# Kernel tuning notes

Measured on AMD Instinct MI355X. Metric: run time of the kernel, lower is better.

## Reference

```python
import jax, jax.numpy as jnp
import numpy as np

HEADS = 8

def _conv(x, w, b, stride, pad):
    # x: [B,C,H,W], w: [O,I,kh,kw] (torch OIHW layout)
    y = jax.lax.conv_general_dilated(x, w, (stride, stride), ((pad, pad), (pad, pad)),
                                     dimension_numbers=('NCHW', 'OIHW', 'NCHW'))
    return y + b[None, :, None, None]

def _maxpool2x2(x):
    # returns pooled values and one-hot argmax per 2x2 window (torch first-max tie-break)
    b, c, H, W = x.shape
    win = x.reshape(b, c, H // 2, 2, W // 2, 2).transpose(0, 1, 2, 4, 3, 5).reshape(b, c, H // 2, W // 2, 4)
    am = jnp.argmax(win, axis=-1)
    oh = jax.nn.one_hot(am, 4, dtype=x.dtype)
    pooled = jnp.sum(win * oh, axis=-1)
    return pooled, oh

def _maxunpool2x2(y, oh):
    b, c, h2, w2 = y.shape
    out = y[..., None] * oh  # [b,c,h2,w2,4]
    out = out.reshape(b, c, h2, w2, 2, 2).transpose(0, 1, 2, 4, 3, 5).reshape(b, c, h2 * 2, w2 * 2)
    return out

def _mha2d(x, wq, wk, wv, wo):
    # x: [b,c,h,w]; wq/wk/wv/wo stored as [in,out] so y = x @ W
    b, c, h, w = x.shape
    hw = h * w
    dk = wq.shape[1]
    dh = dk // HEADS
    xt = x.reshape(b, c, hw).transpose(0, 2, 1)  # [b,hw,c]
    def split(y):  # torch: view(b,hw,dh,heads).permute(0,3,1,2)
        return y.reshape(b, hw, dh, HEADS).transpose(0, 3, 1, 2)  # [b,heads,hw,dh]
    q = split(xt @ wq)
    k = split(xt @ wk)
    v = split(xt @ wv)
    scale = jnp.sqrt(jnp.asarray(dh, x.dtype))
    attn = jax.nn.softmax(jnp.einsum('bhqd,bhkd->bhqk', q, k) / scale, axis=-1)
    o = jnp.einsum('bhqk,bhkd->bhqd', attn, v)
    o = o.transpose(0, 2, 3, 1).reshape(b, hw, dk)  # [b,hw,dh,heads] -> merge
    o = o @ wo
    return o.transpose(0, 2, 1).reshape(b, dk, h, w)

def setup_inputs() -> dict:
    key = jax.random.key(0)
    ks = jax.random.split(key, 10)
    B, C, H, W = 16, 256, 64, 64
    s = 0.05
    return {
        'x': jax.random.normal(ks[0], (B, C, H, W), jnp.float32),
        'conv_w': jax.random.normal(ks[1], (C, C, 3, 3), jnp.float32) * s,
        'conv_b': jax.random.normal(ks[2], (C,), jnp.float32) * s,
        'fr_w': jax.random.normal(ks[3], (C, C, 1, 1), jnp.float32) * s,
        'fr_b': jax.random.normal(ks[4], (C,), jnp.float32) * s,
        'wq': jax.random.normal(ks[5], (C, C), jnp.float32) * s,
        'wk': jax.random.normal(ks[6], (C, C), jnp.float32) * s,
        'wv': jax.random.normal(ks[7], (C, C), jnp.float32) * s,
        'wo': jax.random.normal(ks[8], (C, C), jnp.float32) * s,
        'gamma': jax.random.normal(ks[9], (1,), jnp.float32) * 0.1,
    }

def reference(x, conv_w, conv_b, fr_w, fr_b, wq, wk, wv, wo, gamma):
    _x = _conv(x, fr_w, fr_b, 1, 0)          # 1x1 feature reduction
    _x, oh = _maxpool2x2(_x)                 # MaxPool2d(2, return_indices=True)
    _x = _mha2d(_x, wq, wk, wv, wo)          # attention over pooled grid
    _x = _maxunpool2x2(_x, oh)               # MaxUnpool2d(2)
    return _x * jnp.tanh(gamma[0]) + _conv(x, conv_w, conv_b, 1, 1)
```

## Files before the change

### kernel.cpp

```cpp
#include <hip/hip_runtime.h>
#include <hip/hip_bf16.h>
#include <math.h>

#define B 16
#define C 256
#define H 64
#define W 64
#define H2 32
#define W2 32
#define HW2 1024
#define HEADS 8
#define DH 32

typedef unsigned short ushort_t;
using short8 = __attribute__((ext_vector_type(8))) short;
using u16x8  = __attribute__((ext_vector_type(8))) unsigned short;
using f32x4  = __attribute__((ext_vector_type(4))) float;

__device__ inline ushort_t f2bf(float f) {
    __hip_bfloat16 hb = __float2bfloat16(f);
    return *(ushort_t*)&hb;
}
__device__ inline float bf2f(ushort_t u) {
    return __uint_as_float(((unsigned)u) << 16);
}

__device__ __forceinline__ void cp16(const ushort_t* g, ushort_t* l) {
    __builtin_amdgcn_global_load_lds(
        (const __attribute__((address_space(1))) void*)g,
        (__attribute__((address_space(3))) void*)l, 16, 0, 0);
}

#define RSCALE 0.17677669529663687f

__global__ __launch_bounds__(256) void k_prep_wT(const float* __restrict__ cw,
                                                 ushort_t* __restrict__ wbfT) {
    int i = threadIdx.x, o = blockIdx.x;
    const float* src = cw + ((size_t)o * C + i) * 9;
#pragma unroll
    for (int kk = 0; kk < 9; kk++)
        wbfT[((size_t)kk * C + o) * C + i] = f2bf(src[kk]);
}

__global__ __launch_bounds__(256) void k_prep_wx(
    const float* __restrict__ wq, const float* __restrict__ wk,
    const float* __restrict__ wv, const float* __restrict__ wo,
    const float* __restrict__ frw, ushort_t* __restrict__ wqkvT,
    ushort_t* __restrict__ woT, ushort_t* __restrict__ wfr) {
    int op = blockIdx.x, mat = blockIdx.y, t = threadIdx.x;
    if (mat < 3) {
        const float* w = (mat == 0) ? wq : (mat == 1) ? wk : wv;
        int hh = op >> 5, d = op & 31, col = d * 8 + hh;
        wqkvT[(size_t)mat * 65536 + op * 256 + t] = f2bf(w[t * 256 + col]);
    } else if (mat == 3) {
        int hh = t >> 5, d = t & 31, ic = d * 8 + hh;
        woT[op * 256 + t] = f2bf(wo[ic * 256 + op]);
    } else {
        wfr[op * 256 + t] = f2bf(frw[op * 256 + t]);
    }
}

__global__ __launch_bounds__(256) void k_prep_xn(const float* __restrict__ x,
                                                 ushort_t* __restrict__ xn) {
    __shared__ ushort_t ldsT[64 * 258];
    int t = threadIdx.x;
    int hp = blockIdx.x, b = blockIdx.y;
    ushort_t* dst = xn + ((size_t)(b * 66 + hp)) * 66 * 256;

    if (hp == 0 || hp == 65) {
        u16x8 z = (u16x8){0, 0, 0, 0, 0, 0, 0, 0};
        for (int i = t; i < 2112; i += 256) *(u16x8*)(dst + i * 8) = z;
        return;
    }
    const float* xb = x + ((size_t)b * 256) * 4096 + (size_t)(hp - 1) * 64;
    {
        int cq = t >> 6, w = t & 63;
#pragma unroll 8
        for (int it = 0; it < 64; ++it) {
            int c = it * 4 + cq;
            float v = xb[(size_t)c * 4096 + w];
            ldsT[w * 258 + c] = f2bf(v);
        }
    }
    __syncthreads();
    {
        u16x8 z = (u16x8){0, 0, 0, 0, 0, 0, 0, 0};
        if (t < 32) *(u16x8*)(dst + t * 8) = z;
        else if (t < 64) *(u16x8*)(dst + 65 * 256 + (t - 32) * 8) = z;
    }
    {
        int half = t >> 7, cl = t & 127;
#pragma unroll 4
        for (int it = 0; it < 32; ++it) {
            int w = it * 2 + half;
            unsigned v = *(const unsigned*)&ldsT[w * 258 + cl * 2];
            *(unsigned*)(dst + (size_t)(w + 1) * 256 + cl * 2) = v;
        }
    }
}

__global__ __launch_bounds__(256) void k_conv1pool_mfma(
    const ushort_t* __restrict__ xn, const ushort_t* __restrict__ wfr,
    const float* __restrict__ frb, ushort_t* __restrict__ Pbf,
    unsigned char* __restrict__ idx) {
    __shared__ __align__(16) ushort_t sh[32768];
    ushort_t* Als = sh;
    ushort_t* Bls = sh + 8192;
    int t = threadIdx.x;
    int wg = blockIdx.x;
    int mt = (wg & 7) * 64 + (wg >> 3);
    int b = mt >> 5;
    int h0 = (mt * 2) & 63;

    int r = t >> 2, p = t & 3;
    int kswz = (p ^ ((r >> 1) & 3)) * 8;
    const ushort_t* aB0 = xn + ((size_t)((b * 66 + h0 + 1) * 66 + (r + 1))) * 256 + kswz;
    const ushort_t* aB1 = xn + ((size_t)((b * 66 + h0 + 2) * 66 + (r + 1))) * 256 + kswz;
    const ushort_t* bB = wfr + (size_t)r * 256 + kswz;

    f32x4 acc[4][8];
#pragma unroll
    for (int mf = 0; mf < 4; mf++)
#pragma unroll
        for (int nf = 0; nf < 8; nf++) acc[mf][nf] = (f32x4){0.f, 0.f, 0.f, 0.f};

    cp16(aB0, &Als[t * 8]);
    cp16(aB1, &Als[2048 + t * 8]);
    cp16(bB, &Bls[t * 8]);
    cp16(bB + 64 * 256, &Bls[2048 + t * 8]);
    cp16(bB + 128 * 256, &Bls[4096 + t * 8]);
    cp16(bB + 192 * 256, &Bls[6144 + t * 8]);
    __syncthreads();

    int l = t & 63, wid = t >> 6, wm = wid >> 1, wn = wid & 1;
    int arow = wm * 64 + (l & 15);
    int brow = wn * 128 + (l & 15);
    int pslot = ((l >> 4) ^ ((l >> 1) & 3)) * 8;

    for (int s = 0; s < 8; s++) {
        int cur = s & 1;
        if (s < 7) {
            int off = (s + 1) * 32;
            int nb = cur ^ 1;
            cp16(aB0 + off, &Als[nb * 4096 + t * 8]);
            cp16(aB1 + off, &Als[nb * 4096 + 2048 + t * 8]);
            cp16(bB + off, &Bls[nb * 8192 + t * 8]);
            cp16(bB + 64 * 256 + off, &Bls[nb * 8192 + 2048 + t * 8]);
            cp16(bB + 128 * 256 + off, &Bls[nb * 8192 + 4096 + t * 8]);
            cp16(bB + 192 * 256 + off, &Bls[nb * 8192 + 6144 + t * 8]);
        }
        short8 af[4], bf[8];
#pragma unroll
        for (int mf = 0; mf < 4; mf++)
            af[mf] = *(const short8*)&Als[cur * 4096 + (arow + mf * 16) * 32 + pslot];
#pragma unroll
        for (int nf = 0; nf < 8; nf++)
            bf[nf] = *(const short8*)&Bls[cur * 8192 + (brow + nf * 16) * 32 + pslot];
#pragma unroll
        for (int mf = 0; mf < 4; mf++)
#pragma unroll
            for (int nf = 0; nf < 8; nf++)
                acc[mf][nf] = __builtin_amdgcn_mfma_f32_16x16x32_bf16(
                    af[mf], bf[nf], acc[mf][nf], 0, 0, 0);
        __syncthreads();
    }

#pragma unroll
    for (int nf = 0; nf < 8; nf++) {
        int o = wn * 128 + nf * 16 + (l & 15);
        float bias = frb[o];
#pragma unroll
        for (int mf = 0; mf < 4; mf++) {
            int rbase = wm * 64 + mf * 16 + ((l >> 4) << 2);
            f32x4 a = acc[mf][nf];
#pragma unroll
            for (int jj = 0; jj < 4; jj++)
                sh[(rbase + jj) * 256 + o] = f2bf(a[jj] + bias);
        }
    }
    __syncthreads();

    {
        int h2 = mt & 31;
        size_t rowb = (size_t)(b << 10) + h2 * 32;
        int o0 = (t & 31) * 8;
#pragma unroll
        for (int pp = 0; pp < 4; pp++) {
            int w2 = pp * 8 + (t >> 5);
            u16x8 r0 = *(const u16x8*)&sh[(2 * w2) * 256 + o0];
            u16x8 r1 = *(const u16x8*)&sh[(2 * w2 + 1) * 256 + o0];
            u16x8 r2 = *(const u16x8*)&sh[(64 + 2 * w2) * 256 + o0];
            u16x8 r3 = *(const u16x8*)&sh[(64 + 2 * w2 + 1) * 256 + o0];
            u16x8 pv;
            unsigned amlo = 0, amhi = 0;
#pragma unroll
            for (int e = 0; e < 8; e++) {
                float v0 = bf2f(r0[e]), v1 = bf2f(r1[e]);
                float v2 = bf2f(r2[e]), v3 = bf2f(r3[e]);
                float m = v0;
                ushort_t raw = r0[e];
                unsigned am = 0;
                if (v1 > m) { m = v1; raw = r1[e]; am = 1; }
                if (v2 > m) { m = v2; raw = r2[e]; am = 2; }
                if (v3 > m) { m = v3; raw = r3[e]; am = 3; }
                pv[e] = raw;
                if (e < 4) amlo |= am << (8 * e);
                else       amhi |= am << (8 * (e - 4));
            }
            size_t po = (rowb + w2) * 256 + o0;
            *(u16x8*)(Pbf + po) = pv;
            *(uint2*)(idx + po) = make_uint2(amlo, amhi);
        }
    }
}

__global__ __launch_bounds__(256) void k_qkv_mfma(
    const ushort_t* __restrict__ A, const ushort_t* __restrict__ Bw,
    ushort_t* __restrict__ qb, ushort_t* __restrict__ kb,
    ushort_t* __restrict__ vtb) {
    __shared__ __align__(16) ushort_t Als[2][4096];
    __shared__ __align__(16) ushort_t Bls[2][4096];
    int t = threadIdx.x;
    int wg = blockIdx.x;
    int linear = (wg & 7) * 96 + (wg >> 3);
    int mt = linear / 6, nt = linear % 6;

    int r = t >> 2, p = t & 3;
    int kswz = (p ^ ((r >> 1) & 3)) * 8;
    const ushort_t* aB0 = A + ((size_t)(mt * 128 + r)) * 256 + kswz;
    const ushort_t* aB1 = aB0 + (size_t)64 * 256;
    const ushort_t* bB0 = Bw + ((size_t)(nt * 128 + r)) * 256 + kswz;
    const ushort_t* bB1 = bB0 + (size_t)64 * 256;

    f32x4 acc[4][4];
#pragma unroll
    for (int mf = 0; mf < 4; mf++)
#pragma unroll
        for (int nf = 0; nf < 4; nf++) acc[mf][nf] = (f32x4){0.f, 0.f, 0.f, 0.f};

    cp16(aB0, &Als[0][t * 8]);
    cp16(aB1, &Als[0][2048 + t * 8]);
    cp16(bB0, &Bls[0][t * 8]);
    cp16(bB1, &Bls[0][2048 + t * 8]);
    __syncthreads();

    int l = t & 63, wid = t >> 6, wm = wid >> 1, wn = wid & 1;
    int arow = wm * 64 + (l & 15);
    int brow = wn * 64 + (l & 15);
    int pslot = ((l >> 4) ^ ((l >> 1) & 3)) * 8;

    for (int s = 0; s < 8; s++) {
        int cur = s & 1;
        if (s < 7) {
            int off = (s + 1) * 32;
            int nb = cur ^ 1;
            cp16(aB0 + off, &Als[nb][t * 8]);
            cp16(aB1 + off, &Als[nb][2048 + t * 8]);
            cp16(bB0 + off, &Bls[nb][t * 8]);
            cp16(bB1 + off, &Bls[nb][2048 + t * 8]);
        }
        short8 af[4], bf[4];
#pragma unroll
        for (int mf = 0; mf < 4; mf++)
            af[mf] = *(const short8*)&Als[cur][(arow + mf * 16) * 32 + pslot];
#pragma unroll
        for (int nf = 0; nf < 4; nf++)
            bf[nf] = *(const short8*)&Bls[cur][(brow + nf * 16) * 32 + pslot];
#pragma unroll
        for (int mf = 0; mf < 4; mf++)
#pragma unroll
            for (int nf = 0; nf < 4; nf++)
                acc[mf][nf] = __builtin_amdgcn_mfma_f32_16x16x32_bf16(
                    af[mf], bf[nf], acc[mf][nf], 0, 0, 0);
        __syncthreads();
    }

    if (nt < 4) {
        ushort_t* dst = (nt < 2) ? qb : kb;
        float sc = (nt < 2) ? RSCALE : 1.0f;
        int ccb = (nt & 1) * 128 + wn * 64;
#pragma unroll
        for (int nf = 0; nf < 4; nf++) {
            int cc = ccb + nf * 16 + (l & 15);
#pragma unroll
            for (int mf = 0; mf < 4; mf++) {
                int m = mt * 128 + wm * 64 + mf * 16 + ((l >> 4) << 2);
                f32x4 a = acc[mf][nf];
#pragma unroll
                for (int jj = 0; jj < 4; jj++)
                    dst[(size_t)(m + jj) * 256 + cc] = f2bf(a[jj] * sc);
            }
        }
    } else {
#pragma unroll
        for (int nf = 0; nf < 4; nf++) {
            int cc = (nt & 1) * 128 + wn * 64 + nf * 16 + (l & 15);
#pragma unroll
            for (int mf = 0; mf < 4; mf++) {
                int m = mt * 128 + wm * 64 + mf * 16 + ((l >> 4) << 2);
                int b = m >> 10, n0 = m & 1023;
                f32x4 a = acc[mf][nf];
                unsigned u0 = ((unsigned)f2bf(a[1]) << 16) | f2bf(a[0]);
                unsigned u1 = ((unsigned)f2bf(a[3]) << 16) | f2bf(a[2]);
                *(uint2*)&vtb[((size_t)(b * 256 + cc)) * 1024 + n0] =
                    make_uint2(u0, u1);
            }
        }
    }
}

__global__ __launch_bounds__(256) void k_attn_mfma(
    const ushort_t* __restrict__ qb, const ushort_t* __restrict__ kb,
    const ushort_t* __restrict__ vtb, ushort_t* __restrict__ aoT) {
    __shared__ __align__(16) ushort_t Klds[2][2048];
    __shared__ __align__(16) ushort_t Vlds[2][2048];
    __shared__ __align__(16) ushort_t Plds[4][2304];
    __shared__ float rs_lds[128];

    int t = threadIdx.x;
    int bid = blockIdx.x;
    int swz = (bid & 7) * 128 + (bid >> 3);
    int bh = swz >> 3, qt = swz & 7;
    int b = bh >> 3, h = bh & 7;
    int w = t >> 6, l = t & 63, g = l >> 4, li = l & 15;

    size_t qrow = (size_t)(b * 1024 + qt * 128 + w * 32 + li);
    short8 qv0 = *(const short8*)(qb + qrow * 256 + h * 32 + g * 8);
    short8 qv1 = *(const short8*)(qb + (qrow + 16) * 256 + h * 32 + g * 8);

    int sr = t >> 2, sp = t & 3;
    const ushort_t* kg =
        kb + ((size_t)(b * 1024 + sr)) * 256 + h * 32 + ((sp ^ ((sr >> 1) & 3)) * 8);
    int vd = t >> 3, vs = t & 7;
    const ushort_t* vg =
        vtb + ((size_t)(b * 256 + h * 32 + vd)) * 1024 + ((vs ^ (vd & 7)) * 8);

    f32x4 oacc[2][2];
    f32x4 rsv[2];
#pragma unroll
    for (int qf = 0; qf < 2; qf++) {
        rsv[qf] = (f32x4){0.f, 0.f, 0.f, 0.f};
#pragma unroll
        for (int df = 0; df < 2; df++) oacc[qf][df] = (f32x4){0.f, 0.f, 0.f, 0.f};
    }

    cp16(kg, &Klds[0][t * 8]);
    cp16(vg, &Vlds[0][t * 8]);
    __syncthreads();

    ushort_t* Pw = &Plds[w][0];

    for (int c = 0; c < 16; c++) {
        int cur = c & 1;
        if (c < 15) {
            cp16(kg + (size_t)(c + 1) * 64 * 256, &Klds[cur ^ 1][t * 8]);
            cp16(vg + (c + 1) * 64, &Vlds[cur ^ 1][t * 8]);
        }
        short8 ak[4];
#pragma unroll
        for (int kf = 0; kf < 4; kf++)
            ak[kf] = *(const short8*)&Klds[cur][(16 * kf + li) * 32 +
                                               ((g ^ ((l >> 1) & 3)) * 8)];
#pragma unroll
        for (int qf = 0; qf < 2; qf++) {
            short8 qv = qf ? qv1 : qv0;
#pragma unroll
            for (int kf = 0; kf < 4; kf++) {
                f32x4 st = __builtin_amdgcn_mfma_f32_16x16x32_bf16(
                    ak[kf], qv, (f32x4){0.f, 0.f, 0.f, 0.f}, 0, 0, 0);
                float p0 = __expf(st[0]), p1 = __expf(st[1]);
                float p2 = __expf(st[2]), p3 = __expf(st[3]);
                rsv[qf][0] += p0; rsv[qf][1] += p1;
                rsv[qf][2] += p2; rsv[qf][3] += p3;
                unsigned u0, u1;
                asm("v_cvt_pk_bf16_f32 %0, %1, %2" : "=v"(u0) : "v"(p0), "v"(p1));
                asm("v_cvt_pk_bf16_f32 %0, %1, %2" : "=v"(u1) : "v"(p2), "v"(p3));
                *(uint2*)&Pw[(16 * qf + li) * 72 + 16 * kf + 4 * g] =
                    make_uint2(u0, u1);
            }
        }
#pragma unroll
        for (int win = 0; win < 2; win++) {
            short8 pa[2], bv[2];
#pragma unroll
            for (int qf = 0; qf < 2; qf++)
                pa[qf] = *(const short8*)&Pw[(16 * qf + li) * 72 + win * 32 + 8 * g];
#pragma unroll
            for (int df = 0; df < 2; df++)
                bv[df] = *(const short8*)&Vlds[cur][(16 * df + li) * 64 +
                                                    (((win * 4 + g) ^ (l & 7)) * 8)];
#pragma unroll
            for (int qf = 0; qf < 2; qf++)
#pragma unroll
                for (int df = 0; df < 2; df++)
                    oacc[qf][df] = __builtin_amdgcn_mfma_f32_16x16x32_bf16(
                        pa[qf], bv[df], oacc[qf][df], 0, 0, 0);
        }
        __syncthreads();
    }

#pragma unroll
    for (int qf = 0; qf < 2; qf++) {
        float rs = (rsv[qf][0] + rsv[qf][1]) + (rsv[qf][2] + rsv[qf][3]);
        rs += __shfl_xor(rs, 16);
        rs += __shfl_xor(rs, 32);
        if (l < 16) rs_lds[w * 32 + 16 * qf + li] = rs;
    }
    __syncthreads();

#pragma unroll
    for (int qf = 0; qf < 2; qf++) {
        float4 rs4 = *(const float4*)&rs_lds[w * 32 + 16 * qf + 4 * g];
        float inv[4] = {1.f / rs4.x, 1.f / rs4.y, 1.f / rs4.z, 1.f / rs4.w};
#pragma unroll
        for (int df = 0; df < 2; df++) {
            f32x4 a = oacc[qf][df];
#pragma unroll
            for (int r2 = 0; r2 < 4; r2++) {
                size_t row = (size_t)(b * 1024 + qt * 128 + w * 32 + 16 * qf +
                                      4 * g + r2);
                aoT[row * 256 + h * 32 + 16 * df + li] = f2bf(a[r2] * inv[r2]);
            }
        }
    }
}

__global__ __launch_bounds__(256) void k_oproj_mfma(
    const ushort_t* __restrict__ A, const ushort_t* __restrict__ Bw,
    float* __restrict__ y2) {
    __shared__ __align__(16) ushort_t Als[2][4096];
    __shared__ __align__(16) ushort_t Bls[2][4096];
    int t = threadIdx.x;
    int wg = blockIdx.x;
    int linear = (wg & 7) * 32 + (wg >> 3);
    int nt = linear & 1, mt = linear >> 1;

    int r = t >> 2, p = t & 3;
    int kswz = (p ^ ((r >> 1) & 3)) * 8;
    const ushort_t* aB0 = A + ((size_t)(mt * 128 + r)) * 256 + kswz;
    const ushort_t* aB1 = aB0 + (size_t)64 * 256;
    const ushort_t* bB0 = Bw + ((size_t)(nt * 128 + r)) * 256 + kswz;
    const ushort_t* bB1 = bB0 + (size_t)64 * 256;

    f32x4 acc[4][4];
#pragma unroll
    for (int mf = 0; mf < 4; mf++)
#pragma unroll
        for (int nf = 0; nf < 4; nf++) acc[mf][nf] = (f32x4){0.f, 0.f, 0.f, 0.f};

    cp16(aB0, &Als[0][t * 8]);
    cp16(aB1, &Als[0][2048 + t * 8]);
    cp16(bB0, &Bls[0][t * 8]);
    cp16(bB1, &Bls[0][2048 + t * 8]);
    __syncthreads();

    int l = t & 63, wid = t >> 6, wm = wid >> 1, wn = wid & 1;
    int arow = wm * 64 + (l & 15);
    int brow = wn * 64 + (l & 15);
    int pslot = ((l >> 4) ^ ((l >> 1) & 3)) * 8;

    for (int s = 0; s < 8; s++) {
        int cur = s & 1;
        if (s < 7) {
            int off = (s + 1) * 32;
            int nb = cur ^ 1;
            cp16(aB0 + off, &Als[nb][t * 8]);
            cp16(aB1 + off, &Als[nb][2048 + t * 8]);
            cp16(bB0 + off, &Bls[nb][t * 8]);
            cp16(bB1 + off, &Bls[nb][2048 + t * 8]);
        }
        short8 af[4], bf[4];
#pragma unroll
        for (int mf = 0; mf < 4; mf++)
            af[mf] = *(const short8*)&Als[cur][(arow + mf * 16) * 32 + pslot];
#pragma unroll
        for (int nf = 0; nf < 4; nf++)
            bf[nf] = *(const short8*)&Bls[cur][(brow + nf * 16) * 32 + pslot];
#pragma unroll
        for (int mf = 0; mf < 4; mf++)
#pragma unroll
            for (int nf = 0; nf < 4; nf++)
                acc[mf][nf] = __builtin_amdgcn_mfma_f32_16x16x32_bf16(
                    af[mf], bf[nf], acc[mf][nf], 0, 0, 0);
        __syncthreads();
    }

#pragma unroll
    for (int nf = 0; nf < 4; nf++) {
        int cc = nt * 128 + wn * 64 + nf * 16 + (l & 15);
#pragma unroll
        for (int mf = 0; mf < 4; mf++) {
            int m = mt * 128 + wm * 64 + mf * 16 + ((l >> 4) << 2);
            f32x4 a = acc[mf][nf];
#pragma unroll
            for (int jj = 0; jj < 4; jj++)
                y2[(size_t)(m + jj) * 256 + cc] = a[jj];
        }
    }
}

__global__ __launch_bounds__(512) void k_conv3_mfma(
    const ushort_t* __restrict__ xn, const ushort_t* __restrict__ wbfT,
    const float* __restrict__ cb, const float* __restrict__ y2,
    const unsigned char* __restrict__ idx, const float* __restrict__ gamma,
    float* __restrict__ out) {
    extern __shared__ __align__(16) ushort_t lds[];
    ushort_t* AL = lds;
    ushort_t* BL = lds + 32768;
    int t = threadIdx.x;
    int mt = blockIdx.x;

    int srow = t >> 3, sslot = t & 7;
    int kel = (sslot ^ (srow & 7)) * 8;
    const ushort_t* aP[2][2];
    const ushort_t* bP[2][2];
#pragma unroll
    for (int hf = 0; hf < 2; hf++)
#pragma unroll
        for (int j = 0; j < 2; j++) {
            int row = hf * 128 + j * 64 + srow;
            int m = mt * 256 + row;
            int b0 = m >> 12, h0 = (m >> 6) & 63, w0 = m & 63;
            aP[hf][j] = xn + ((size_t)((b0 * 66 + h0) * 66 + w0)) * 256 + kel;
            bP[hf][j] = wbfT + (size_t)row * 256 + kel;
        }

    auto offA = [](int kt) -> int {
        int it = kt / 9, khkw = kt - it * 9;
        int kh = khkw / 3, kw = khkw - kh * 3;
        return (kh * 66 + kw) * 256 + it * 64;
    };
    auto offB = [](int kt) -> int {
        int it = kt / 9, khkw = kt - it * 9;
        return khkw * 65536 + it * 64;
    };
    auto STAGE_A = [&](int bb, int hf, int kt) {
        int o = offA(kt);
        ushort_t* d = AL + bb * 16384 + hf * 8192 + t * 8;
        cp16(aP[hf][0] + o, d);
        cp16(aP[hf][1] + o, d + 4096);
    };
    auto STAGE_B = [&](int bb, int hf, int kt) {
        int o = offB(kt);
        ushort_t* d = BL + bb * 16384 + hf * 8192 + t * 8;
        cp16(bP[hf][0] + o, d);
        cp16(bP[hf][1] + o, d + 4096);
    };

    f32x4 acc[8][4];
#pragma unroll
    for (int mf = 0; mf < 8; mf++)
#pragma unroll
        for (int nf = 0; nf < 4; nf++) acc[mf][nf] = (f32x4){0.f, 0.f, 0.f, 0.f};

    int l = t & 63, wid = t >> 6, wm = wid >> 2, wn = wid & 3;
    int lr = l & 15, g = l >> 4, l7 = l & 7;
    int abase = wm * 8192;
    int bbase = (wn >> 1) * 8192 + (wn & 1) * 4096;

    short8 Xa[4][2], Xb[2][2], Ya[4][2], Yb[2][2];

    auto READF = [&](short8 (&fa)[4][2], short8 (&fb)[2][2],
                     const ushort_t* Ab, const ushort_t* Bb, int ah, int bh) {
#pragma unroll
        for (int mf = 0; mf < 4; mf++)
#pragma unroll
            for (int kk = 0; kk < 2; kk++)
                fa[mf][kk] = *(const short8*)
                    &Ab[(ah * 64 + mf * 16 + lr) * 64 + (((kk * 4 + g) ^ l7) * 8)];
#pragma unroll
        for (int nf = 0; nf < 2; nf++)
#pragma unroll
            for (int kk = 0; kk < 2; kk++)
                fb[nf][kk] = *(const short8*)
                    &Bb[(bh * 32 + nf * 16 + lr) * 64 + (((kk * 4 + g) ^ l7) * 8)];
    };
    auto MFMAQ = [&](short8 (&fa)[4][2], short8 (&fb)[2][2], int mo, int no) {
        __builtin_amdgcn_s_setprio(1);
#pragma unroll
        for (int kk = 0; kk < 2; kk++)
#pragma unroll
            for (int mf = 0; mf < 4; mf++)
#pragma unroll
                for (int nf = 0; nf < 2; nf++)
                    acc[mf + mo][nf + no] = __builtin_amdgcn_mfma_f32_16x16x32_bf16(
                        fa[mf][kk], fb[nf][kk], acc[mf + mo][nf + no], 0, 0, 0);
        __builtin_amdgcn_s_setprio(0);
    };
    auto BARW = [&]() {
        __builtin_amdgcn_sched_barrier(0);
        __builtin_amdgcn_s_barrier();
        __builtin_amdgcn_sched_barrier(0);
    };

    STAGE_A(0, 0, 0); STAGE_A(0, 1, 0); STAGE_B(0, 0, 0); STAGE_B(0, 1, 0);
    asm volatile("s_waitcnt vmcnt(0)" ::: "memory");
    STAGE_B(1, 0, 1); STAGE_B(1, 1, 1);
    __builtin_amdgcn_s_barrier();
    READF(Xa, Xb, AL + abase, BL + bbase, 0, 0);

    for (int kt = 0; kt < 36; kt++) {
        int cur = kt & 1, nxt = cur ^ 1;
        const ushort_t* Ac = AL + cur * 16384 + abase;
        const ushort_t* Bc = BL + cur * 16384 + bbase;
        BARW();
        if (kt < 35) { STAGE_A(nxt, 0, kt + 1); STAGE_A(nxt, 1, kt + 1); }
        READF(Ya, Yb, Ac, Bc, 0, 1);
        MFMAQ(Xa, Xb, 0, 0);
        BARW();
        READF(Xa, Xb, Ac, Bc, 1, 1);
        MFMAQ(Ya, Yb, 0, 2);
        BARW();
        asm volatile("s_waitcnt vmcnt(0)" ::: "memory");
        READF(Ya, Yb, Ac, Bc, 1, 0);
        MFMAQ(Xa, Xb, 4, 2);
        BARW();
        if (kt < 34) { STAGE_B(cur, 0, kt + 2); STAGE_B(cur, 1, kt + 2); }
        if (kt < 35) {
            const ushort_t* An = AL + nxt * 16384 + abase;
            const ushort_t* Bn = BL + nxt * 16384 + bbase;
            READF(Xa, Xb, An, Bn, 0, 0);
        }
        MFMAQ(Ya, Yb, 4, 0);
    }

    float tg = tanhf(gamma[0]);
    int mbase = mt * 256 + wm * 128 + (g << 2);
    int obase = wn * 64 + lr;
#pragma unroll
    for (int nf = 0; nf < 4; nf++) {
        int o = obase + nf * 16;
        float bias = cb[o];
#pragma unroll
        for (int mf = 0; mf < 8; mf++) {
            int m = mbase + mf * 16;
            int b = m >> 12, h = (m >> 6) & 63, w0 = m & 63;
            const unsigned char* idr = idx + ((size_t)(b << 10)) * 256;
            const float* y2r = y2 + ((size_t)(b << 10)) * 256;
            f32x4 a = acc[mf][nf];
            float v4[4];
#pragma unroll
            for (int jj = 0; jj < 4; jj++) {
                int wj = w0 + jj;
                int n2 = ((h >> 1) << 5) + (wj >> 1);
                int j2 = ((h & 1) << 1) + (wj & 1);
                float val = a[jj] + bias;
                if (idr[(size_t)n2 * 256 + o] == (unsigned char)j2)
                    val += tg * y2r[(size_t)n2 * 256 + o];
                v4[jj] = val;
            }
            *(float4*)(out + (((size_t)(b * C + o) * H + h) << 6) + w0) =
                make_float4(v4[0], v4[1], v4[2], v4[3]);
        }
    }
}

extern "C" void kernel_launch(void* const* d_in, const int* in_sizes, int n_in,
                              void* d_out, int out_size, void* d_ws, size_t ws_size,
                              hipStream_t stream) {
    const float* x      = (const float*)d_in[0];
    const float* conv_w = (const float*)d_in[1];
    const float* conv_b = (const float*)d_in[2];
    const float* fr_w   = (const float*)d_in[3];
    const float* fr_b   = (const float*)d_in[4];
    const float* wq     = (const float*)d_in[5];
    const float* wk     = (const float*)d_in[6];
    const float* wv     = (const float*)d_in[7];
    const float* wo     = (const float*)d_in[8];
    const float* gamma  = (const float*)d_in[9];
    float* out = (float*)d_out;
    char* ws = (char*)d_ws;

    ushort_t* wbfT  = (ushort_t*)(ws + 0);
    ushort_t* wfrbf = (ushort_t*)(ws + 1179648);
    ushort_t* wqkvT = (ushort_t*)(ws + 1310720);
    ushort_t* woT   = (ushort_t*)(ws + 1703936);
    ushort_t* xn    = (ushort_t*)(ws + 2097152);
    ushort_t* Pbf   = (ushort_t*)(ws + 37781504);
    unsigned char* idx = (unsigned char*)(ws + 46170112);
    ushort_t* qb    = (ushort_t*)(ws + 50364416);
    ushort_t* kb    = (ushort_t*)(ws + 58753024);
    ushort_t* vtb   = (ushort_t*)(ws + 67141632);
    ushort_t* aoT   = (ushort_t*)(ws + 75530240);
    float* y2       = (float*)(ws + 50364416);

    k_prep_wT<<<dim3(C), dim3(256), 0, stream>>>(conv_w, wbfT);
    k_prep_wx<<<dim3(256, 5), dim3(256), 0, stream>>>(wq, wk, wv, wo, fr_w,
                                                      wqkvT, woT, wfrbf);
    k_prep_xn<<<dim3(66, B), dim3(256), 0, stream>>>(x, xn);
    k_conv1pool_mfma<<<dim3(512), dim3(256), 0, stream>>>(xn, wfrbf, fr_b, Pbf, idx);
    k_qkv_mfma<<<dim3(768), dim3(256), 0, stream>>>(Pbf, wqkvT, qb, kb, vtb);
    k_attn_mfma<<<dim3(1024), dim3(256), 0, stream>>>(qb, kb, vtb, aoT);
    k_oproj_mfma<<<dim3(256), dim3(256), 0, stream>>>(aoT, woT, y2);
    (void)hipFuncSetAttribute(reinterpret_cast<const void*>(k_conv3_mfma),
                              hipFuncAttributeMaxDynamicSharedMemorySize, 131072);
    k_conv3_mfma<<<dim3(256), dim3(512), 131072, stream>>>(xn, wbfT, conv_b, y2, idx,
                                                           gamma, out);
    (void)in_sizes; (void)n_in; (void)out_size; (void)ws_size;
}
```

Measured before the change: 224.6 us.

## Restructure conv GEMM main loop into two half-phases with full B fragments

Rewrites the K-loop of the 3x3 conv implicit GEMM so each iteration has two phases instead of four. Each phase loads one half of the A fragments and all of the B fragments for the wave, cutting barriers per K-tile from four to two. The staging order changes too: A tiles are now prefetched two steps ahead and B tiles one step ahead, the reverse of before. Holding both A halves and both B halves raises register pressure, and each barrier now covers more MFMA and LDS work.

```diff
diff --git a/kernel.cpp b/kernel.cpp
--- a/kernel.cpp
+++ b/kernel.cpp
@@ -558,16 +558,17 @@
     int abase = wm * 8192;
     int bbase = (wn >> 1) * 8192 + (wn & 1) * 4096;
 
-    short8 Xa[4][2], Xb[2][2], Ya[4][2], Yb[2][2];
-
-    auto READF = [&](short8 (&fa)[4][2], short8 (&fb)[2][2],
-                     const ushort_t* Ab, const ushort_t* Bb, int ah, int bh) {
+    short8 aLo[4][2], aHi[4][2], bf0[2][2], bf1[2][2];
+
+    auto RD_A = [&](short8 (&fa)[4][2], const ushort_t* Ab, int ah) {
 #pragma unroll
         for (int mf = 0; mf < 4; mf++)
 #pragma unroll
             for (int kk = 0; kk < 2; kk++)
                 fa[mf][kk] = *(const short8*)
                     &Ab[(ah * 64 + mf * 16 + lr) * 64 + (((kk * 4 + g) ^ l7) * 8)];
+    };
+    auto RD_B = [&](short8 (&fb)[2][2], const ushort_t* Bb, int bh) {
 #pragma unroll
         for (int nf = 0; nf < 2; nf++)
 #pragma unroll
@@ -575,7 +576,7 @@
                 fb[nf][kk] = *(const short8*)
                     &Bb[(bh * 32 + nf * 16 + lr) * 64 + (((kk * 4 + g) ^ l7) * 8)];
     };
-    auto MFMAQ = [&](short8 (&fa)[4][2], short8 (&fb)[2][2], int mo, int no) {
+    auto MFMAH = [&](short8 (&fa)[4][2], int mo) {
         __builtin_amdgcn_s_setprio(1);
 #pragma unroll
         for (int kk = 0; kk < 2; kk++)
@@ -583,8 +584,16 @@
             for (int mf = 0; mf < 4; mf++)
 #pragma unroll
                 for (int nf = 0; nf < 2; nf++)
-                    acc[mf + mo][nf + no] = __builtin_amdgcn_mfma_f32_16x16x32_bf16(
-                        fa[mf][kk], fb[nf][kk], acc[mf + mo][nf + no], 0, 0, 0);
+                    acc[mf + mo][nf] = __builtin_amdgcn_mfma_f32_16x16x32_bf16(
+                        fa[mf][kk], bf0[nf][kk], acc[mf + mo][nf], 0, 0, 0);
+#pragma unroll
+        for (int kk = 0; kk < 2; kk++)
+#pragma unroll
+            for (int mf = 0; mf < 4; mf++)
+#pragma unroll
+                for (int nf = 0; nf < 2; nf++)
+                    acc[mf + mo][nf + 2] = __builtin_amdgcn_mfma_f32_16x16x32_bf16(
+                        fa[mf][kk], bf1[nf][kk], acc[mf + mo][nf + 2], 0, 0, 0);
         __builtin_amdgcn_s_setprio(0);
     };
     auto BARW = [&]() {
@@ -594,34 +603,28 @@
     };
 
     STAGE_A(0, 0, 0); STAGE_A(0, 1, 0); STAGE_B(0, 0, 0); STAGE_B(0, 1, 0);
-    asm volatile("s_waitcnt vmcnt(0)" ::: "memory");
-    STAGE_B(1, 0, 1); STAGE_B(1, 1, 1);
+    STAGE_A(1, 0, 1); STAGE_A(1, 1, 1);
+    asm volatile("s_waitcnt vmcnt(4)" ::: "memory");
     __builtin_amdgcn_s_barrier();
-    READF(Xa, Xb, AL + abase, BL + bbase, 0, 0);
+    RD_A(aLo, AL + abase, 0);
+    RD_B(bf0, BL + bbase, 0);
+    RD_B(bf1, BL + bbase, 1);
 
     for (int kt = 0; kt < 36; kt++) {
         int cur = kt & 1, nxt = cur ^ 1;
         const ushort_t* Ac = AL + cur * 16384 + abase;
-        const ushort_t* Bc = BL + cur * 16384 + bbase;
+        const ushort_t* An = AL + nxt * 16384 + abase;
+        const ushort_t* Bn = BL + nxt * 16384 + bbase;
         BARW();
-        if (kt < 35) { STAGE_A(nxt, 0, kt + 1); STAGE_A(nxt, 1, kt + 1); }
-        READF(Ya, Yb, Ac, Bc, 0, 1);
-        MFMAQ(Xa, Xb, 0, 0);
+        if (kt < 35) { STAGE_B(nxt, 0, kt + 1); STAGE_B(nxt, 1, kt + 1); }
+        RD_A(aHi, Ac, 1);
+        MFMAH(aLo, 0);
+        asm volatile("s_waitcnt vmcnt(0)" ::: "memory");
         BARW();
-        READF(Xa, Xb, Ac, Bc, 1, 1);
-        MFMAQ(Ya, Yb, 0, 2);
-        BARW();
-        asm volatile("s_waitcnt vmcnt(0)" ::: "memory");
-        READF(Ya, Yb, Ac, Bc, 1, 0);
-        MFMAQ(Xa, Xb, 4, 2);
-        BARW();
-        if (kt < 34) { STAGE_B(cur, 0, kt + 2); STAGE_B(cur, 1, kt + 2); }
-        if (kt < 35) {
-            const ushort_t* An = AL + nxt * 16384 + abase;
-            const ushort_t* Bn = BL + nxt * 16384 + bbase;
-            READF(Xa, Xb, An, Bn, 0, 0);
-        }
-        MFMAQ(Ya, Yb, 4, 0);
+        if (kt < 34) { STAGE_A(cur, 0, kt + 2); STAGE_A(cur, 1, kt + 2); }
+        if (kt < 35) RD_A(aLo, An, 0);
+        MFMAH(aHi, 4);
+        if (kt < 35) { RD_B(bf0, Bn, 0); RD_B(bf1, Bn, 1); }
     }
 
     float tg = tanhf(gamma[0]);
```

After: 218.0 us. -3.0%, faster.
